# Optimization experiments

Hardware: AMD Instinct MI355X
Metric: run time of the kernel (lower is better)

## Reference

```python
import jax, jax.numpy as jnp
import numpy as np

IN_FEATURES = 4096
OUT_FEATURES = 4096
MIN_PREC = 3   # min(precisions)
MAXMEM = 6
BL, BH = 4, 5  # floor/ceil of p = sigmoid(0)*3 + 3 = 4.5 (static, matches p.item() usage)


def dequant_kbit(qweight, lut, b):
    """Bitplane LUT dequant: qweight (P, O, IN//32) int32, lut (O, 2**b) -> (O, IN) float.
    Plane j holds one bit per weight (32 weights packed per int32, LSB-first within
    the int32); the first b planes form the b-bit code, plane 0 being the MSB."""
    planes = qweight[:b]                                   # (b, O, IN//32)
    shifts = jnp.arange(32, dtype=jnp.int32)               # bit position within int32
    bits = (planes[..., None] >> shifts) & 1               # (b, O, IN//32, 32)
    bits = bits.reshape(b, planes.shape[1], -1)            # (b, O, IN)
    weights = (jnp.arange(b, dtype=jnp.int32)[::-1])[:, None, None]  # MSB-first
    code = jnp.sum(bits << weights, axis=0)                # (O, IN) int32 in [0, 2**b)
    return jnp.take_along_axis(lut, code, axis=1)          # (O, IN)


def setup_inputs() -> dict:
    key = jax.random.key(0)
    k_x, k_q, k_l4, k_l5, k_b = jax.random.split(key, 5)
    x = jax.random.normal(k_x, (4, 2048, IN_FEATURES), dtype=jnp.float32)
    z = jnp.float32(0.0)  # z_inv = log(z_init/(1-z_init)) with z_init=0.5
    qweight = jax.random.randint(k_q, (MAXMEM, OUT_FEATURES, IN_FEATURES // 32),
                                 minval=-(2**31), maxval=2**31 - 1, dtype=jnp.int32)
    # LUTs: sorted quantization levels per output row (realistic for quantized linear)
    lut4 = jnp.sort(0.02 * jax.random.normal(k_l4, (OUT_FEATURES, 2**BL), dtype=jnp.float32), axis=-1)
    lut5 = jnp.sort(0.02 * jax.random.normal(k_l5, (OUT_FEATURES, 2**BH), dtype=jnp.float32), axis=-1)
    bias = 0.01 * jax.random.normal(k_b, (OUT_FEATURES,), dtype=jnp.float32)
    return {"x": x, "z": z, "lut4": lut4, "lut5": lut5, "bias": bias, "qweight": qweight}


def reference(x, z, lut4, lut5, bias, qweight):
    prange_len = MAXMEM - MIN_PREC
    p = jax.nn.sigmoid(z) * prange_len + MIN_PREC   # 4.5 at init
    r = 1.0 - (p - BL)                              # blend weight for low-bit branch
    wl = dequant_kbit(qweight, lut4, BL)            # (O, IN)
    wh = dequant_kbit(qweight, lut5, BH)            # (O, IN)
    yl = jnp.einsum('bsi,oi->bso', x, wl)
    yh = jnp.einsum('bsi,oi->bso', x, wh)
    return yl * r + yh * (1.0 - r) + bias
```

## Files before the change

### kernel.cpp

```cpp
#include <hip/hip_runtime.h>
#include <hip/hip_bf16.h>


#define IN_F   4096
#define OUT_F  4096
#define M_DIM  8192

#define CAST_BLOCKS 8192
#define DEQ_BLOCKS  2048

#define NT (IN_F / 64)

typedef __bf16          bf16x8   __attribute__((ext_vector_type(8)));
typedef float           f32x4    __attribute__((ext_vector_type(4)));
typedef unsigned short  ushortx8 __attribute__((ext_vector_type(8)));

__device__ __forceinline__ unsigned short f32_to_bf16(float f) {
    unsigned int u = __builtin_bit_cast(unsigned int, f);
    u += 0x7fffu + ((u >> 16) & 1u);
    return (unsigned short)(u >> 16);
}

__device__ __forceinline__ void async_load16(const void* g, void* l) {
    __builtin_amdgcn_global_load_lds(
        (const __attribute__((address_space(1))) unsigned int*)g,
        (__attribute__((address_space(3))) unsigned int*)l,
        16, 0, 0);
}

__device__ __forceinline__ void stage_half(const unsigned short* g0,
                                           unsigned short* l0) {
    async_load16(g0, l0);
    async_load16(g0 + (size_t)64 * IN_F, l0 + 4096);
}

__global__ __launch_bounds__(256) void prologue_kernel(
    const float* __restrict__ x,
    const unsigned int* __restrict__ qw,
    const float* __restrict__ lut4,
    const float* __restrict__ lut5,
    const float* __restrict__ zp,
    unsigned short* __restrict__ xb,
    unsigned short* __restrict__ W)
{
    const int tid = threadIdx.x;

    if (blockIdx.x < CAST_BLOCKS) {
        const size_t i = (size_t)blockIdx.x * 4096 + (size_t)tid * 16;
        const f32x4* src = (const f32x4*)(x + i);
        f32x4 a0 = src[0], a1 = src[1], a2 = src[2], a3 = src[3];
        ushortx8 o0, o1;
        #pragma unroll
        for (int e = 0; e < 4; ++e) {
            o0[e]     = f32_to_bf16(a0[e]);
            o0[4 + e] = f32_to_bf16(a1[e]);
            o1[e]     = f32_to_bf16(a2[e]);
            o1[4 + e] = f32_to_bf16(a3[e]);
        }
        ushortx8* dst = (ushortx8*)(xb + i);
        dst[0] = o0;
        dst[1] = o1;
        return;
    }

    __shared__ float sc[2][32];
    const int bid = blockIdx.x - CAST_BLOCKS;
    const int o0 = bid * 2;

    if (tid < 64) {
        const float z   = zp[0];
        const float sig = 1.0f / (1.0f + __expf(-z));
        const float r   = 2.0f - 3.0f * sig;
        const float ri  = 1.0f - r;
        const int row = tid >> 5;
        const int c   = tid & 31;
        sc[row][c] = r * lut4[(o0 + row) * 16 + (c >> 1)]
                   + ri * lut5[(o0 + row) * 32 + c];
    }
    __syncthreads();

    const int gid = bid * 256 + tid;
    const int lo  = (gid >> 7) & 1;

    const int PS = OUT_F * (IN_F / 32);
    const unsigned int q0 = qw[0 * PS + gid];
    const unsigned int q1 = qw[1 * PS + gid];
    const unsigned int q2 = qw[2 * PS + gid];
    const unsigned int q3 = qw[3 * PS + gid];
    const unsigned int q4 = qw[4 * PS + gid];

    unsigned short outv[32];
    #pragma unroll
    for (int i = 0; i < 32; ++i) {
        const unsigned c5 = (((q0 >> i) & 1u) << 4) | (((q1 >> i) & 1u) << 3) |
                            (((q2 >> i) & 1u) << 2) | (((q3 >> i) & 1u) << 1) |
                             ((q4 >> i) & 1u);
        outv[i] = f32_to_bf16(sc[lo][c5]);
    }

    ushortx8* dst = (ushortx8*)(W + (size_t)gid * 32);
    #pragma unroll
    for (int j = 0; j < 4; ++j) {
        ushortx8 v;
        #pragma unroll
        for (int e = 0; e < 8; ++e) v[e] = outv[j * 8 + e];
        dst[j] = v;
    }
}


#define MFMA_BF16 __builtin_amdgcn_mfma_f32_16x16x32_bf16

__device__ __forceinline__ void tile_step(
    int t,
    const unsigned short* cA, unsigned short* cB, unsigned short* nA,
    int tid,
    const unsigned short* gA0, const unsigned short* gA1,
    const unsigned short* gB0, const unsigned short* gB1,
    int aBase, int bBase, int ck0, int ck1,
    f32x4 (&acc)[8][4])
{
    bf16x8 af[4], bf0[4], bf1[4];

    #pragma unroll
    for (int m = 0; m < 4; ++m)
        af[m] = *(const bf16x8*)(cA + aBase + m * 1024 + ck0);
    #pragma unroll
    for (int n = 0; n < 4; ++n)
        bf0[n] = *(const bf16x8*)(cB + bBase + n * 1024 + ck0);
    if (t + 1 < NT) stage_half(gA0 + (size_t)(t + 1) * 64, nA + tid * 8);
    __builtin_amdgcn_s_barrier();
    asm volatile("s_waitcnt lgkmcnt(0)" ::: "memory");
    __builtin_amdgcn_sched_barrier(0);
    __builtin_amdgcn_s_setprio(1);
    #pragma unroll
    for (int m = 0; m < 4; ++m)
        #pragma unroll
        for (int n = 0; n < 4; ++n)
            acc[m][n] = MFMA_BF16(af[m], bf0[n], acc[m][n], 0, 0, 0);
    __builtin_amdgcn_s_setprio(0);
    __builtin_amdgcn_sched_barrier(0);
    __builtin_amdgcn_s_barrier();

    #pragma unroll
    for (int m = 0; m < 4; ++m)
        af[m] = *(const bf16x8*)(cA + aBase + m * 1024 + ck1);
    #pragma unroll
    for (int n = 0; n < 4; ++n)
        bf1[n] = *(const bf16x8*)(cB + bBase + n * 1024 + ck1);
    if (t + 1 < NT) stage_half(gA1 + (size_t)(t + 1) * 64, nA + 8192 + tid * 8);
    __builtin_amdgcn_s_barrier();
    asm volatile("s_waitcnt lgkmcnt(0)" ::: "memory");
    __builtin_amdgcn_sched_barrier(0);
    __builtin_amdgcn_s_setprio(1);
    #pragma unroll
    for (int m = 0; m < 4; ++m)
        #pragma unroll
        for (int n = 0; n < 4; ++n)
            acc[m][n] = MFMA_BF16(af[m], bf1[n], acc[m][n], 0, 0, 0);
    __builtin_amdgcn_s_setprio(0);
    __builtin_amdgcn_sched_barrier(0);
    __builtin_amdgcn_s_barrier();

    #pragma unroll
    for (int m = 0; m < 4; ++m)
        af[m] = *(const bf16x8*)(cA + aBase + (m + 4) * 1024 + ck0);
    if (t + 2 < NT) stage_half(gB0 + (size_t)(t + 2) * 64, cB + tid * 8);
    __builtin_amdgcn_s_barrier();
    asm volatile("s_waitcnt lgkmcnt(0)" ::: "memory");
    __builtin_amdgcn_sched_barrier(0);
    __builtin_amdgcn_s_setprio(1);
    #pragma unroll
    for (int m = 0; m < 4; ++m)
        #pragma unroll
        for (int n = 0; n < 4; ++n)
            acc[m + 4][n] = MFMA_BF16(af[m], bf0[n], acc[m + 4][n], 0, 0, 0);
    __builtin_amdgcn_s_setprio(0);
    __builtin_amdgcn_sched_barrier(0);
    __builtin_amdgcn_s_barrier();

    #pragma unroll
    for (int m = 0; m < 4; ++m)
        af[m] = *(const bf16x8*)(cA + aBase + (m + 4) * 1024 + ck1);
    if (t + 2 < NT) stage_half(gB1 + (size_t)(t + 2) * 64, cB + 8192 + tid * 8);
    if (t < NT - 2) asm volatile("s_waitcnt vmcnt(4)" ::: "memory");
    else            asm volatile("s_waitcnt vmcnt(0)" ::: "memory");
    __builtin_amdgcn_s_barrier();
    asm volatile("s_waitcnt lgkmcnt(0)" ::: "memory");
    __builtin_amdgcn_sched_barrier(0);
    __builtin_amdgcn_s_setprio(1);
    #pragma unroll
    for (int m = 0; m < 4; ++m)
        #pragma unroll
        for (int n = 0; n < 4; ++n)
            acc[m + 4][n] = MFMA_BF16(af[m], bf1[n], acc[m + 4][n], 0, 0, 0);
    __builtin_amdgcn_s_setprio(0);
    __builtin_amdgcn_sched_barrier(0);
    __builtin_amdgcn_s_barrier();
}

__global__ __launch_bounds__(512, 2) void gemm_bt_kernel(
    const unsigned short* __restrict__ A,
    const unsigned short* __restrict__ B,
    const float* __restrict__ bias,
    float* __restrict__ C)
{
    __shared__ unsigned short sA[2][256 * 64];
    __shared__ unsigned short sB[2][256 * 64];

    const int tid = threadIdx.x;

    const int id  = blockIdx.x;
    const int swz = (id & 7) * 64 + (id >> 3);
    const int bn  = swz & 15;
    const int bm  = swz >> 4;

    const int l   = tid & 63;
    const int wv  = tid >> 6;
    const int wr  = wv >> 2;
    const int wc  = wv & 3;
    const int l15 = l & 15;
    const int q   = l >> 4;
    const int xm  = l15 & 7;

    const int aBase = (wr * 128 + l15) * 64;
    const int bBase = (wc * 64  + l15) * 64;
    const int ck0   = ((q)     ^ xm) * 8;
    const int ck1   = ((4 + q) ^ xm) * 8;

    const int r  = tid >> 3;
    const int cx = ((tid & 7) ^ (r & 7)) * 8;
    const unsigned short* gA0 = A + (size_t)(bm * 256 + r) * IN_F + cx;
    const unsigned short* gA1 = gA0 + (size_t)128 * IN_F;
    const unsigned short* gB0 = B + (size_t)(bn * 256 + r) * IN_F + cx;
    const unsigned short* gB1 = gB0 + (size_t)128 * IN_F;

    stage_half(gB0,      &sB[0][0] + tid * 8);
    stage_half(gB1,      &sB[0][0] + 8192 + tid * 8);
    stage_half(gA0,      &sA[0][0] + tid * 8);
    stage_half(gA1,      &sA[0][0] + 8192 + tid * 8);
    stage_half(gB0 + 64, &sB[1][0] + tid * 8);
    stage_half(gB1 + 64, &sB[1][0] + 8192 + tid * 8);
    asm volatile("s_waitcnt vmcnt(4)" ::: "memory");
    __builtin_amdgcn_s_barrier();

    f32x4 acc[8][4] = {};

    #pragma unroll 1
    for (int tp = 0; tp < NT; tp += 2) {
        tile_step(tp,     &sA[0][0], &sB[0][0], &sA[1][0], tid,
                  gA0, gA1, gB0, gB1, aBase, bBase, ck0, ck1, acc);
        tile_step(tp + 1, &sA[1][0], &sB[1][0], &sA[0][0], tid,
                  gA0, gA1, gB0, gB1, aBase, bBase, ck0, ck1, acc);
    }

    const int row0 = bm * 256 + wr * 128 + q * 4;
    const int col0 = bn * 256 + wc * 64 + l15;
    #pragma unroll
    for (int n = 0; n < 4; ++n) {
        const float bv = bias[col0 + n * 16];
        #pragma unroll
        for (int m = 0; m < 8; ++m) {
            #pragma unroll
            for (int rr = 0; rr < 4; ++rr)
                C[(size_t)(row0 + m * 16 + rr) * OUT_F + (col0 + n * 16)] =
                    acc[m][n][rr] + bv;
        }
    }
}

extern "C" void kernel_launch(void* const* d_in, const int* in_sizes, int n_in,
                              void* d_out, int out_size, void* d_ws, size_t ws_size,
                              hipStream_t stream)
{
    const float*        x    = (const float*)d_in[0];
    const float*        z    = (const float*)d_in[1];
    const float*        lut4 = (const float*)d_in[2];
    const float*        lut5 = (const float*)d_in[3];
    const float*        bias = (const float*)d_in[4];
    const unsigned int* qw   = (const unsigned int*)d_in[5];
    float* out = (float*)d_out;

    unsigned short* xb = (unsigned short*)d_ws;
    unsigned short* wb = xb + (size_t)M_DIM * IN_F;

    prologue_kernel<<<CAST_BLOCKS + DEQ_BLOCKS, 256, 0, stream>>>(
        x, qw, lut4, lut5, z, xb, wb);
    gemm_bt_kernel<<<(M_DIM / 256) * (OUT_F / 256), 512, 0, stream>>>(
        xb, wb, bias, out);
}
```

Baseline: 481.7 us.

## Collapse per-step GEMM barriers from eight to two and batch fragment loads

Restructures the bf16 MFMA tile step so both B fragment halves are read once at the start. Each pair of MFMA groups now runs back to back, with only two workgroup barriers per step instead of eight, and no explicit LDS waits. The async global-to-LDS staging is grouped into pairs issued before each MFMA block, and the prologue load order puts A first. The aim is to cut barrier and wait stalls and give the scheduler more overlap between LDS reads and MFMAs. In exchange, more fragments are live at once, which raises register pressure under the 512-thread, two-block launch bound.

```diff
diff --git a/kernel.cpp b/kernel.cpp
--- a/kernel.cpp
+++ b/kernel.cpp
@@ -10,6 +10,7 @@
 #define DEQ_BLOCKS  2048
 
 #define NT (IN_F / 64)
+#define TSH (256 * 64)
 
 typedef __bf16          bf16x8   __attribute__((ext_vector_type(8)));
 typedef float           f32x4    __attribute__((ext_vector_type(4)));
@@ -120,83 +121,81 @@
     int aBase, int bBase, int ck0, int ck1,
     f32x4 (&acc)[8][4])
 {
-    bf16x8 af[4], bf0[4], bf1[4];
-
-    #pragma unroll
-    for (int m = 0; m < 4; ++m)
-        af[m] = *(const bf16x8*)(cA + aBase + m * 1024 + ck0);
+    bf16x8 bf0[4], bf1[4], afa[4], afb[4], afc[4], afd[4];
+
     #pragma unroll
     for (int n = 0; n < 4; ++n)
         bf0[n] = *(const bf16x8*)(cB + bBase + n * 1024 + ck0);
-    if (t + 1 < NT) stage_half(gA0 + (size_t)(t + 1) * 64, nA + tid * 8);
-    __builtin_amdgcn_s_barrier();
-    asm volatile("s_waitcnt lgkmcnt(0)" ::: "memory");
-    __builtin_amdgcn_sched_barrier(0);
-    __builtin_amdgcn_s_setprio(1);
-    #pragma unroll
-    for (int m = 0; m < 4; ++m)
-        #pragma unroll
-        for (int n = 0; n < 4; ++n)
-            acc[m][n] = MFMA_BF16(af[m], bf0[n], acc[m][n], 0, 0, 0);
-    __builtin_amdgcn_s_setprio(0);
-    __builtin_amdgcn_sched_barrier(0);
-    __builtin_amdgcn_s_barrier();
-
-    #pragma unroll
-    for (int m = 0; m < 4; ++m)
-        af[m] = *(const bf16x8*)(cA + aBase + m * 1024 + ck1);
     #pragma unroll
     for (int n = 0; n < 4; ++n)
         bf1[n] = *(const bf16x8*)(cB + bBase + n * 1024 + ck1);
-    if (t + 1 < NT) stage_half(gA1 + (size_t)(t + 1) * 64, nA + 8192 + tid * 8);
+    #pragma unroll
+    for (int m = 0; m < 4; ++m)
+        afa[m] = *(const bf16x8*)(cA + aBase + m * 1024 + ck0);
+
+    if (t + 1 < NT) {
+        stage_half(gA0 + (size_t)(t + 1) * 64, nA + tid * 8);
+        stage_half(gA1 + (size_t)(t + 1) * 64, nA + 8192 + tid * 8);
+    }
+
+    __builtin_amdgcn_s_setprio(1);
+    #pragma unroll
+    for (int m = 0; m < 4; ++m)
+        #pragma unroll
+        for (int n = 0; n < 4; ++n)
+            acc[m][n] = MFMA_BF16(afa[m], bf0[n], acc[m][n], 0, 0, 0);
+    __builtin_amdgcn_s_setprio(0);
+
+    #pragma unroll
+    for (int m = 0; m < 4; ++m)
+        afb[m] = *(const bf16x8*)(cA + aBase + m * 1024 + ck1);
+
+    __builtin_amdgcn_s_setprio(1);
+    #pragma unroll
+    for (int m = 0; m < 4; ++m)
+        #pragma unroll
+        for (int n = 0; n < 4; ++n)
+            acc[m][n] = MFMA_BF16(afb[m], bf1[n], acc[m][n], 0, 0, 0);
+    __builtin_amdgcn_s_setprio(0);
+
+    __builtin_amdgcn_sched_barrier(0);
     __builtin_amdgcn_s_barrier();
-    asm volatile("s_waitcnt lgkmcnt(0)" ::: "memory");
-    __builtin_amdgcn_sched_barrier(0);
-    __builtin_amdgcn_s_setprio(1);
-    #pragma unroll
-    for (int m = 0; m < 4; ++m)
-        #pragma unroll
-        for (int n = 0; n < 4; ++n)
-            acc[m][n] = MFMA_BF16(af[m], bf1[n], acc[m][n], 0, 0, 0);
-    __builtin_amdgcn_s_setprio(0);
-    __builtin_amdgcn_sched_barrier(0);
-    __builtin_amdgcn_s_barrier();
-
-    #pragma unroll
-    for (int m = 0; m < 4; ++m)
-        af[m] = *(const bf16x8*)(cA + aBase + (m + 4) * 1024 + ck0);
-    if (t + 2 < NT) stage_half(gB0 + (size_t)(t + 2) * 64, cB + tid * 8);
-    __builtin_amdgcn_s_barrier();
-    asm volatile("s_waitcnt lgkmcnt(0)" ::: "memory");
-    __builtin_amdgcn_sched_barrier(0);
-    __builtin_amdgcn_s_setprio(1);
-    #pragma unroll
-    for (int m = 0; m < 4; ++m)
-        #pragma unroll
-        for (int n = 0; n < 4; ++n)
-            acc[m + 4][n] = MFMA_BF16(af[m], bf0[n], acc[m + 4][n], 0, 0, 0);
-    __builtin_amdgcn_s_setprio(0);
-    __builtin_amdgcn_sched_barrier(0);
-    __builtin_amdgcn_s_barrier();
-
-    #pragma unroll
-    for (int m = 0; m < 4; ++m)
-        af[m] = *(const bf16x8*)(cA + aBase + (m + 4) * 1024 + ck1);
-    if (t + 2 < NT) stage_half(gB1 + (size_t)(t + 2) * 64, cB + 8192 + tid * 8);
+    __builtin_amdgcn_sched_barrier(0);
+
+    #pragma unroll
+    for (int m = 0; m < 4; ++m)
+        afc[m] = *(const bf16x8*)(cA + aBase + (m + 4) * 1024 + ck0);
+
+    if (t + 2 < NT) {
+        stage_half(gB0 + (size_t)(t + 2) * 64, cB + tid * 8);
+        stage_half(gB1 + (size_t)(t + 2) * 64, cB + 8192 + tid * 8);
+    }
+
+    __builtin_amdgcn_s_setprio(1);
+    #pragma unroll
+    for (int m = 0; m < 4; ++m)
+        #pragma unroll
+        for (int n = 0; n < 4; ++n)
+            acc[m + 4][n] = MFMA_BF16(afc[m], bf0[n], acc[m + 4][n], 0, 0, 0);
+    __builtin_amdgcn_s_setprio(0);
+
+    #pragma unroll
+    for (int m = 0; m < 4; ++m)
+        afd[m] = *(const bf16x8*)(cA + aBase + (m + 4) * 1024 + ck1);
+
+    __builtin_amdgcn_s_setprio(1);
+    #pragma unroll
+    for (int m = 0; m < 4; ++m)
+        #pragma unroll
+        for (int n = 0; n < 4; ++n)
+            acc[m + 4][n] = MFMA_BF16(afd[m], bf1[n], acc[m + 4][n], 0, 0, 0);
+    __builtin_amdgcn_s_setprio(0);
+
+    __builtin_amdgcn_sched_barrier(0);
     if (t < NT - 2) asm volatile("s_waitcnt vmcnt(4)" ::: "memory");
     else            asm volatile("s_waitcnt vmcnt(0)" ::: "memory");
     __builtin_amdgcn_s_barrier();
-    asm volatile("s_waitcnt lgkmcnt(0)" ::: "memory");
-    __builtin_amdgcn_sched_barrier(0);
-    __builtin_amdgcn_s_setprio(1);
-    #pragma unroll
-    for (int m = 0; m < 4; ++m)
-        #pragma unroll
-        for (int n = 0; n < 4; ++n)
-            acc[m + 4][n] = MFMA_BF16(af[m], bf1[n], acc[m + 4][n], 0, 0, 0);
-    __builtin_amdgcn_s_setprio(0);
-    __builtin_amdgcn_sched_barrier(0);
-    __builtin_amdgcn_s_barrier();
+    __builtin_amdgcn_sched_barrier(0);
 }
 
 __global__ __launch_bounds__(512, 2) void gemm_bt_kernel(
@@ -205,8 +204,8 @@
     const float* __restrict__ bias,
     float* __restrict__ C)
 {
-    __shared__ unsigned short sA[2][256 * 64];
-    __shared__ unsigned short sB[2][256 * 64];
+    __shared__ unsigned short sA[2][TSH];
+    __shared__ unsigned short sB[2][TSH];
 
     const int tid = threadIdx.x;
 
@@ -235,14 +234,15 @@
     const unsigned short* gB0 = B + (size_t)(bn * 256 + r) * IN_F + cx;
     const unsigned short* gB1 = gB0 + (size_t)128 * IN_F;
 
+    stage_half(gA0,      &sA[0][0] + tid * 8);
+    stage_half(gA1,      &sA[0][0] + 8192 + tid * 8);
     stage_half(gB0,      &sB[0][0] + tid * 8);
     stage_half(gB1,      &sB[0][0] + 8192 + tid * 8);
-    stage_half(gA0,      &sA[0][0] + tid * 8);
-    stage_half(gA1,      &sA[0][0] + 8192 + tid * 8);
     stage_half(gB0 + 64, &sB[1][0] + tid * 8);
     stage_half(gB1 + 64, &sB[1][0] + 8192 + tid * 8);
     asm volatile("s_waitcnt vmcnt(4)" ::: "memory");
     __builtin_amdgcn_s_barrier();
+    __builtin_amdgcn_sched_barrier(0);
 
     f32x4 acc[8][4] = {};
 
```

Measured after the change: 467.8 us. -2.9%, faster.
